# Performance work log

Measured on AMD Instinct MI355X. Metric: run time of the kernel, lower is better.

## Reference

```python
import jax, jax.numpy as jnp
import numpy as np

N_EMBD = 384
HEAD_SIZE = 64
BLOCK_SIZE = 64
SCALE = HEAD_SIZE * N_EMBD ** (-0.5)  # non-standard scale from source: k.shape[-1] * C**-0.5


def setup_inputs() -> dict:
    key = jax.random.key(0)
    kx, kk, kq, kv = jax.random.split(key, 4)
    B, T = 2048, BLOCK_SIZE
    x = jax.random.normal(kx, (B, T, N_EMBD), dtype=jnp.float32)
    # torch Linear(n_embd, head_size, bias=False): weight shape [head_size, n_embd], y = x @ W.T
    s = N_EMBD ** -0.5
    Wk = jax.random.uniform(kk, (HEAD_SIZE, N_EMBD), jnp.float32, -s, s)
    Wq = jax.random.uniform(kq, (HEAD_SIZE, N_EMBD), jnp.float32, -s, s)
    Wv = jax.random.uniform(kv, (HEAD_SIZE, N_EMBD), jnp.float32, -s, s)
    return {"x": x, "Wk": Wk, "Wq": Wq, "Wv": Wv}


def reference(x, Wk, Wq, Wv) -> jnp.ndarray:
    B, T, C = x.shape
    k = jnp.einsum("btc,hc->bth", x, Wk)  # [B,T,H]
    q = jnp.einsum("btc,hc->bth", x, Wq)
    v = jnp.einsum("btc,hc->bth", x, Wv)
    wei = jnp.einsum("bth,bsh->bts", q, k) * SCALE  # [B,T,T]
    causal = jnp.tril(jnp.ones((T, T), dtype=bool))
    wei = jnp.where(causal, wei, -jnp.inf)
    wei = jax.nn.softmax(wei, axis=-1)
    out = jnp.einsum("bts,bsh->bth", wei, v)  # [B,T,H]
    return out
```

## Files before the change

kernel.cpp:

```cpp
#include <hip/hip_runtime.h>

typedef _Float16 f16;
typedef _Float16 f16x8 __attribute__((ext_vector_type(8)));
typedef _Float16 f16x4 __attribute__((ext_vector_type(4)));
typedef float    f32x4 __attribute__((ext_vector_type(4)));

#define MFMA16(a, b, c) __builtin_amdgcn_mfma_f32_16x16x32_f16((a), (b), (c), 0, 0, 0)

constexpr int T = 64;
constexpr int C = 384;
constexpr int H = 64;
constexpr float SCALE = 3.26598632371090f;

__device__ __forceinline__ void load_lds16(const float* g, float* l) {
  __builtin_amdgcn_global_load_lds(
      (const __attribute__((address_space(1))) void*)g,
      (__attribute__((address_space(3))) void*)l, 16, 0, 0);
}

__global__ void pack_w(const float* __restrict__ Wk, const float* __restrict__ Wq,
                       const float* __restrict__ Wv, f16* __restrict__ Wp) {
  int tid = blockIdx.x * blockDim.x + threadIdx.x;
  if (tid >= 3 * 12 * 4 * 64) return;
  int lane = tid & 63;
  int tile = tid >> 6;
  int ht = tile & 3;
  int kt = (tile >> 2) % 12;
  int wi = tile / 48;
  const float* W = (wi == 0) ? Wk : ((wi == 1) ? Wq : Wv);
  int h = 16 * ht + (lane & 15);
  int c = 32 * kt + 8 * (lane >> 4);
  const float* src = W + h * C + c;
  f16x8 v;
#pragma unroll
  for (int j = 0; j < 8; ++j) v[j] = (f16)src[j];
  *(f16x8*)(Wp + (size_t)tile * 512 + lane * 8) = v;
}

__global__ __launch_bounds__(256, 3) void head_fused(
    const float* __restrict__ x, const f16* __restrict__ Wp,
    float* __restrict__ out) {
  __shared__ float xc[3][2048];
  __shared__ f16 qp_lds[64][72];
  __shared__ f16 k_lds[64][72];
  __shared__ f16 vT_lds[64][72];

  const int b = blockIdx.x;
  const int tid = threadIdx.x;
  const int w = tid >> 6;
  const int lane = tid & 63;
  const int l15 = lane & 15;
  const int g = lane >> 4;
  const int t_ = 16 * w + l15;

  const f32x4 vzero = {0.0f, 0.0f, 0.0f, 0.0f};
  f32x4 acc[3][4];
#pragma unroll
  for (int c = 0; c < 3; ++c)
#pragma unroll
    for (int tt = 0; tt < 4; ++tt) acc[c][tt] = vzero;

  const f16* wp_base[3];
  bool isV[3];
#pragma unroll
  for (int c = 0; c < 3; ++c) {
    int combo = 3 * w + c;
    int m = combo >> 2;
    int ht = combo & 3;
    wp_base[c] = Wp + (size_t)(m * 48 + ht) * 512 + lane * 8;
    isV[c] = (combo >= 8);
  }

  const float* xbase = x + (size_t)b * T * C;
  const float* gsrc = xbase + (size_t)(16 * w + l15) * C + g * 8;

  load_lds16(gsrc + 0 * 32 + 0, &xc[0][(2 * w + 0) * 256]);
  load_lds16(gsrc + 0 * 32 + 4, &xc[0][(2 * w + 1) * 256]);
  load_lds16(gsrc + 1 * 32 + 0, &xc[1][(2 * w + 0) * 256]);
  load_lds16(gsrc + 1 * 32 + 4, &xc[1][(2 * w + 1) * 256]);
  f16x8 wpc[3], wpn[3];
#pragma unroll
  for (int c = 0; c < 3; ++c) wpc[c] = *(const f16x8*)(wp_base[c]);

#pragma unroll
  for (int kt = 0; kt < 12; ++kt) {
    const int cur = kt % 3;
    if (kt == 0)      __builtin_amdgcn_s_waitcnt(0x0070);
    else if (kt < 11) __builtin_amdgcn_s_waitcnt(0x0075);
    else              __builtin_amdgcn_s_waitcnt(0x0073);
    __builtin_amdgcn_s_barrier();

    if (kt + 1 < 12) {
#pragma unroll
      for (int c = 0; c < 3; ++c)
        wpn[c] = *(const f16x8*)(wp_base[c] + (size_t)(kt + 1) * 2048);
    }
    if (kt + 2 < 12) {
      const int nb = (kt + 2) % 3;
      load_lds16(gsrc + (kt + 2) * 32 + 0, &xc[nb][(2 * w + 0) * 256]);
      load_lds16(gsrc + (kt + 2) * 32 + 4, &xc[nb][(2 * w + 1) * 256]);
    }

    f16x8 xf[4];
#pragma unroll
    for (int tt = 0; tt < 4; ++tt) {
      f32x4 A0 = *(const f32x4*)&xc[cur][(2 * tt + 0) * 256 + lane * 4];
      f32x4 A1 = *(const f32x4*)&xc[cur][(2 * tt + 1) * 256 + lane * 4];
#pragma unroll
      for (int j = 0; j < 4; ++j) { xf[tt][j] = (f16)A0[j]; xf[tt][4 + j] = (f16)A1[j]; }
    }
#pragma unroll
    for (int c = 0; c < 3; ++c) {
      f16x8 wf = wpc[c];
      if (!isV[c]) {
#pragma unroll
        for (int tt = 0; tt < 4; ++tt) acc[c][tt] = MFMA16(wf, xf[tt], acc[c][tt]);
      } else {
#pragma unroll
        for (int tt = 0; tt < 4; ++tt) acc[c][tt] = MFMA16(xf[tt], wf, acc[c][tt]);
      }
      wpc[c] = wpn[c];
    }
  }

#pragma unroll
  for (int c = 0; c < 3; ++c) {
    int combo = 3 * w + c;
    int m = combo >> 2;
    int ht = combo & 3;
#pragma unroll
    for (int tt = 0; tt < 4; ++tt) {
      f16x4 pd;
#pragma unroll
      for (int r = 0; r < 4; ++r) pd[r] = (f16)acc[c][tt][r];
      if (m == 0) {
        *(f16x4*)&k_lds[16 * tt + l15][16 * ht + 4 * g] = pd;
      } else if (m == 1) {
        *(f16x4*)&qp_lds[16 * tt + l15][16 * ht + 4 * g] = pd;
      } else {
        *(f16x4*)&vT_lds[16 * ht + l15][16 * tt + 4 * g] = pd;
      }
    }
  }
  __syncthreads();

  f32x4 accs[4];
#pragma unroll
  for (int i = 0; i < 4; ++i) accs[i] = vzero;
#pragma unroll
  for (int kt = 0; kt < 2; ++kt) {
    f16x8 qf = *(const f16x8*)&qp_lds[t_][32 * kt + 8 * g];
#pragma unroll
    for (int mt = 0; mt < 4; ++mt) {
      f16x8 kf = *(const f16x8*)&k_lds[16 * mt + l15][32 * kt + 8 * g];
      accs[mt] = MFMA16(kf, qf, accs[mt]);
    }
  }

  float e[16];
  float mx = -__builtin_inff();
#pragma unroll
  for (int mt = 0; mt < 4; ++mt) {
#pragma unroll
    for (int r = 0; r < 4; ++r) {
      int s = 16 * mt + 4 * g + r;
      float lv = accs[mt][r] * SCALE;
      lv = (s <= t_) ? lv : -__builtin_inff();
      e[mt * 4 + r] = lv;
      mx = fmaxf(mx, lv);
    }
  }
  mx = fmaxf(mx, __shfl_xor(mx, 16));
  mx = fmaxf(mx, __shfl_xor(mx, 32));
  float sm = 0.0f;
#pragma unroll
  for (int i = 0; i < 16; ++i) { e[i] = __expf(e[i] - mx); sm += e[i]; }
  sm += __shfl_xor(sm, 16);
  sm += __shfl_xor(sm, 32);
  const float inv = 1.0f / sm;
#pragma unroll
  for (int mt = 0; mt < 4; ++mt) {
    f16x4 pp;
#pragma unroll
    for (int r = 0; r < 4; ++r) pp[r] = (f16)(e[mt * 4 + r] * inv);
    *(f16x4*)&qp_lds[t_][16 * mt + 4 * g] = pp;
  }

  f32x4 acco[4];
#pragma unroll
  for (int i = 0; i < 4; ++i) acco[i] = vzero;
#pragma unroll
  for (int kt = 0; kt < 2; ++kt) {
    f16x8 pf = *(const f16x8*)&qp_lds[t_][32 * kt + 8 * g];
#pragma unroll
    for (int mt = 0; mt < 4; ++mt) {
      f16x8 vf = *(const f16x8*)&vT_lds[16 * mt + l15][32 * kt + 8 * g];
      acco[mt] = MFMA16(vf, pf, acco[mt]);
    }
  }

  float* orow = out + ((size_t)b * T + t_) * H;
#pragma unroll
  for (int mt = 0; mt < 4; ++mt) {
    *(f32x4*)(orow + 16 * mt + 4 * g) = acco[mt];
  }
}

extern "C" void kernel_launch(void* const* d_in, const int* in_sizes, int n_in,
                              void* d_out, int out_size, void* d_ws, size_t ws_size,
                              hipStream_t stream) {
  const float* x  = (const float*)d_in[0];
  const float* Wk = (const float*)d_in[1];
  const float* Wq = (const float*)d_in[2];
  const float* Wv = (const float*)d_in[3];
  float* out = (float*)d_out;
  f16* Wp = (f16*)d_ws;

  pack_w<<<36, 256, 0, stream>>>(Wk, Wq, Wv, Wp);
  head_fused<<<2048, 256, 0, stream>>>(x, Wp, out);
}
```

Before: 302.3 us.

## Double K-step per pipeline stage, repack weights, alias LDS buffers

The projection loop now processes 64 channels per barrier stage instead of 32, halving the number of barriers and waits. Each stage issues twice as many global-to-LDS loads and weight loads. Weights are repacked so that all tiles for one K-step are contiguous. The x staging buffer is aliased with the q/k/vT LDS buffers, with a barrier added before reuse. Explicit vmcnt waits and sched_barriers enforce the schedule. The larger per-stage buffer, at 48KB LDS, may reduce occupancy relative to the launch bounds target.

```diff
diff --git a/kernel.cpp b/kernel.cpp
--- a/kernel.cpp
+++ b/kernel.cpp
@@ -34,16 +34,19 @@
   f16x8 v;
 #pragma unroll
   for (int j = 0; j < 8; ++j) v[j] = (f16)src[j];
-  *(f16x8*)(Wp + (size_t)tile * 512 + lane * 8) = v;
+  int tile2 = kt * 12 + wi * 4 + ht;
+  *(f16x8*)(Wp + (size_t)tile2 * 512 + lane * 8) = v;
 }
 
 __global__ __launch_bounds__(256, 3) void head_fused(
     const float* __restrict__ x, const f16* __restrict__ Wp,
     float* __restrict__ out) {
-  __shared__ float xc[3][2048];
-  __shared__ f16 qp_lds[64][72];
-  __shared__ f16 k_lds[64][72];
-  __shared__ f16 vT_lds[64][72];
+  __shared__ __attribute__((aligned(16))) char smem[49152];
+  float* xcf = (float*)smem;
+  typedef f16 row72[72];
+  row72* qp_lds = (row72*)smem;
+  row72* k_lds  = (row72*)(smem + 9216);
+  row72* vT_lds = (row72*)(smem + 18432);
 
   const int b = blockIdx.x;
   const int tid = threadIdx.x;
@@ -65,63 +68,91 @@
 #pragma unroll
   for (int c = 0; c < 3; ++c) {
     int combo = 3 * w + c;
-    int m = combo >> 2;
-    int ht = combo & 3;
-    wp_base[c] = Wp + (size_t)(m * 48 + ht) * 512 + lane * 8;
+    wp_base[c] = Wp + (size_t)combo * 512 + lane * 8;
     isV[c] = (combo >= 8);
   }
 
   const float* xbase = x + (size_t)b * T * C;
-  const float* gsrc = xbase + (size_t)(16 * w + l15) * C + g * 8;
-
-  load_lds16(gsrc + 0 * 32 + 0, &xc[0][(2 * w + 0) * 256]);
-  load_lds16(gsrc + 0 * 32 + 4, &xc[0][(2 * w + 1) * 256]);
-  load_lds16(gsrc + 1 * 32 + 0, &xc[1][(2 * w + 0) * 256]);
-  load_lds16(gsrc + 1 * 32 + 4, &xc[1][(2 * w + 1) * 256]);
-  f16x8 wpc[3], wpn[3];
-#pragma unroll
-  for (int c = 0; c < 3; ++c) wpc[c] = *(const f16x8*)(wp_base[c]);
-
-#pragma unroll
-  for (int kt = 0; kt < 12; ++kt) {
+  const float* gsrc = xbase + (size_t)(16 * w + l15) * C + 8 * g;
+
+#pragma unroll
+  for (int kh = 0; kh < 2; ++kh)
+#pragma unroll
+    for (int hf = 0; hf < 2; ++hf)
+      load_lds16(gsrc + kh * 32 + hf * 4, &xcf[0 * 4096 + kh * 2048 + (2 * w + hf) * 256]);
+  f16x8 wpc[3][2], wpn[3][2];
+#pragma unroll
+  for (int c = 0; c < 3; ++c)
+#pragma unroll
+    for (int kh = 0; kh < 2; ++kh)
+      wpc[c][kh] = *(const f16x8*)(wp_base[c] + (size_t)(0 * 2 + kh) * 6144);
+  __builtin_amdgcn_sched_barrier(0);
+#pragma unroll
+  for (int kh = 0; kh < 2; ++kh)
+#pragma unroll
+    for (int hf = 0; hf < 2; ++hf)
+      load_lds16(gsrc + 64 + kh * 32 + hf * 4, &xcf[1 * 4096 + kh * 2048 + (2 * w + hf) * 256]);
+
+#pragma unroll
+  for (int kt = 0; kt < 6; ++kt) {
     const int cur = kt % 3;
-    if (kt == 0)      __builtin_amdgcn_s_waitcnt(0x0070);
-    else if (kt < 11) __builtin_amdgcn_s_waitcnt(0x0075);
-    else              __builtin_amdgcn_s_waitcnt(0x0073);
+    if (kt < 5) {
+      asm volatile("s_waitcnt vmcnt(10)" ::: "memory");
+    } else {
+      asm volatile("s_waitcnt vmcnt(6)" ::: "memory");
+    }
+    __builtin_amdgcn_sched_barrier(0);
     __builtin_amdgcn_s_barrier();
-
-    if (kt + 1 < 12) {
+    __builtin_amdgcn_sched_barrier(0);
+
+    if (kt + 1 < 6) {
 #pragma unroll
       for (int c = 0; c < 3; ++c)
-        wpn[c] = *(const f16x8*)(wp_base[c] + (size_t)(kt + 1) * 2048);
-    }
-    if (kt + 2 < 12) {
+#pragma unroll
+        for (int kh = 0; kh < 2; ++kh)
+          wpn[c][kh] = *(const f16x8*)(wp_base[c] + (size_t)((kt + 1) * 2 + kh) * 6144);
+    }
+    __builtin_amdgcn_sched_barrier(0);
+    if (kt + 2 < 6) {
       const int nb = (kt + 2) % 3;
-      load_lds16(gsrc + (kt + 2) * 32 + 0, &xc[nb][(2 * w + 0) * 256]);
-      load_lds16(gsrc + (kt + 2) * 32 + 4, &xc[nb][(2 * w + 1) * 256]);
-    }
-
-    f16x8 xf[4];
-#pragma unroll
-    for (int tt = 0; tt < 4; ++tt) {
-      f32x4 A0 = *(const f32x4*)&xc[cur][(2 * tt + 0) * 256 + lane * 4];
-      f32x4 A1 = *(const f32x4*)&xc[cur][(2 * tt + 1) * 256 + lane * 4];
-#pragma unroll
-      for (int j = 0; j < 4; ++j) { xf[tt][j] = (f16)A0[j]; xf[tt][4 + j] = (f16)A1[j]; }
-    }
-#pragma unroll
-    for (int c = 0; c < 3; ++c) {
-      f16x8 wf = wpc[c];
-      if (!isV[c]) {
-#pragma unroll
-        for (int tt = 0; tt < 4; ++tt) acc[c][tt] = MFMA16(wf, xf[tt], acc[c][tt]);
-      } else {
-#pragma unroll
-        for (int tt = 0; tt < 4; ++tt) acc[c][tt] = MFMA16(xf[tt], wf, acc[c][tt]);
+#pragma unroll
+      for (int kh = 0; kh < 2; ++kh)
+#pragma unroll
+        for (int hf = 0; hf < 2; ++hf)
+          load_lds16(gsrc + (kt + 2) * 64 + kh * 32 + hf * 4,
+                     &xcf[nb * 4096 + kh * 2048 + (2 * w + hf) * 256]);
+    }
+    __builtin_amdgcn_sched_barrier(0);
+
+#pragma unroll
+    for (int kh = 0; kh < 2; ++kh) {
+      f16x8 xf[4];
+#pragma unroll
+      for (int tt = 0; tt < 4; ++tt) {
+        f32x4 A0 = *(const f32x4*)&xcf[cur * 4096 + kh * 2048 + (2 * tt + 0) * 256 + lane * 4];
+        f32x4 A1 = *(const f32x4*)&xcf[cur * 4096 + kh * 2048 + (2 * tt + 1) * 256 + lane * 4];
+#pragma unroll
+        for (int j = 0; j < 4; ++j) { xf[tt][j] = (f16)A0[j]; xf[tt][4 + j] = (f16)A1[j]; }
       }
-      wpc[c] = wpn[c];
-    }
-  }
+#pragma unroll
+      for (int c = 0; c < 3; ++c) {
+        f16x8 wf = wpc[c][kh];
+        if (!isV[c]) {
+#pragma unroll
+          for (int tt = 0; tt < 4; ++tt) acc[c][tt] = MFMA16(wf, xf[tt], acc[c][tt]);
+        } else {
+#pragma unroll
+          for (int tt = 0; tt < 4; ++tt) acc[c][tt] = MFMA16(xf[tt], wf, acc[c][tt]);
+        }
+      }
+    }
+#pragma unroll
+    for (int c = 0; c < 3; ++c)
+#pragma unroll
+      for (int kh = 0; kh < 2; ++kh) wpc[c][kh] = wpn[c][kh];
+  }
+
+  __builtin_amdgcn_s_barrier();
 
 #pragma unroll
   for (int c = 0; c < 3; ++c) {
```

Result: no change. 297.1 us (-1.7%).
